# Optimization experiments

Hardware: AMD Instinct MI355X
Metric: run time of the kernel (lower is better)

## Reference

```python
import jax, jax.numpy as jnp
import numpy as np

N_EMB = 384
BLOCK_SIZE = 256


def setup_inputs() -> dict:
    key = jax.random.key(0)
    ks = jax.random.split(key, 6)
    B, T, H, D = 256, 256, 6, 64
    x = jax.random.normal(ks[0], (B, T, N_EMB), dtype=jnp.float32)
    wk = jax.random.normal(ks[1], (H, N_EMB, D), dtype=jnp.float32) * (N_EMB ** -0.5)
    wq = jax.random.normal(ks[2], (H, N_EMB, D), dtype=jnp.float32) * (N_EMB ** -0.5)
    wv = jax.random.normal(ks[3], (H, N_EMB, D), dtype=jnp.float32) * (N_EMB ** -0.5)
    wproj = jax.random.normal(ks[4], (N_EMB, N_EMB), dtype=jnp.float32) * (N_EMB ** -0.5)
    bproj = jnp.zeros((N_EMB,), dtype=jnp.float32)
    return {"x": x, "wk": wk, "wq": wq, "wv": wv, "wproj": wproj, "bproj": bproj}


def reference(x, wk, wq, wv, wproj, bproj):
    B, T, C = x.shape  # C == N_EMB
    # per-head projections (no bias), heads stacked on leading axis
    k = jnp.einsum('btc,hcd->bhtd', x, wk)
    q = jnp.einsum('btc,hcd->bhtd', x, wq)
    v = jnp.einsum('btc,hcd->bhtd', x, wv)
    # faithful to source: wei = k @ q^T scaled by sqrt(C) (embed dim, not head dim)
    wei = jnp.einsum('bhtd,bhsd->bhts', k, q) / (C ** 0.5)
    causal = jnp.tril(jnp.ones((T, T), dtype=bool))
    wei = jnp.where(causal, wei, -jnp.inf)
    wei = jax.nn.softmax(wei, axis=-1)
    # dropout is identity in eval mode
    out = jnp.einsum('bhts,bhsd->bhtd', wei, v)  # [B,H,T,D]
    out = out.transpose(0, 2, 1, 3).reshape(B, T, C)  # concat heads
    out = out @ wproj + bproj
    return out
```

## Files before the change

### kernel.cpp

```cpp
#include <hip/hip_runtime.h>

typedef unsigned short u16;
typedef __bf16 bf16x8 __attribute__((ext_vector_type(8)));
typedef float f32x4 __attribute__((ext_vector_type(4)));

#define B_SZ 256
#define T_SZ 256
#define C_EMB 384
#define NHEAD 6
#define DHEAD 64
#define N3 1152
#define BHTD 25165824
#define SCALE 0.05103103630798287f

__device__ __forceinline__ u16 f2bf(float f) {
  unsigned u = __float_as_uint(f);
  u += 0x7FFFu + ((u >> 16) & 1u);
  return (u16)(u >> 16);
}

__device__ __forceinline__ void gload_lds16(const void* g, void* l) {
  __builtin_amdgcn_global_load_lds((const __attribute__((address_space(1))) void*)g,
                                   (__attribute__((address_space(3))) void*)l, 16, 0, 0);
}

__global__ __launch_bounds__(256) void prep_weights(
    const float* __restrict__ wk, const float* __restrict__ wq,
    const float* __restrict__ wv, const float* __restrict__ wproj,
    u16* __restrict__ wqkvt, u16* __restrict__ wprojt) {
  int i = blockIdx.x * 256 + threadIdx.x;
  if (i < N3 * C_EMB) {
    int n = i / C_EMB, c = i - n * C_EMB;
    int tensor = n >= 768 ? 2 : (n >= 384 ? 1 : 0);
    int r = n - tensor * 384;
    int h = r >> 6, d = r & 63;
    const float* w = tensor == 0 ? wk : (tensor == 1 ? wq : wv);
    float val = w[(h * C_EMB + c) * DHEAD + d];
    if (tensor == 0) val *= SCALE;
    wqkvt[i] = f2bf(val);
  } else {
    int ii = i - N3 * C_EMB;
    if (ii < C_EMB * C_EMB) {
      int n = ii / C_EMB, c = ii - n * C_EMB;
      wprojt[ii] = f2bf(wproj[c * C_EMB + n]);
    }
  }
}

__global__ __launch_bounds__(256) void prep_x(const float* __restrict__ x,
                                              u16* __restrict__ xb) {
  int i = blockIdx.x * 256 + threadIdx.x;
  float4 f0 = ((const float4*)x)[i * 2];
  float4 f1 = ((const float4*)x)[i * 2 + 1];
  uint4 p;
  p.x = (unsigned)f2bf(f0.x) | ((unsigned)f2bf(f0.y) << 16);
  p.y = (unsigned)f2bf(f0.z) | ((unsigned)f2bf(f0.w) << 16);
  p.z = (unsigned)f2bf(f1.x) | ((unsigned)f2bf(f1.y) << 16);
  p.w = (unsigned)f2bf(f1.z) | ((unsigned)f2bf(f1.w) << 16);
  ((uint4*)xb)[i] = p;
}

__global__ __launch_bounds__(256) void qkv_gemm(const u16* __restrict__ xb,
                                                const u16* __restrict__ wt,
                                                u16* __restrict__ kqv) {
  __shared__ __align__(16) u16 lA[2][128 * 64];
  __shared__ __align__(16) u16 lB[2][128 * 64];
  const int tid = threadIdx.x;
  const int lane = tid & 63, w = tid >> 6;
  int bid = blockIdx.x;
  int nb = (bid & 7) * 576 + (bid >> 3);
  int mt = nb / 9, nt = nb - mt * 9;
  const int n0 = nt * 128, m0 = mt * 128;
  const int wr = w >> 1, wc = w & 1;
  f32x4 acc[4][4] = {};

#define QSTAGE(buf, kt_) { \
    int k0_ = (kt_) * 64; \
    _Pragma("unroll") for (int it = 0; it < 4; ++it) { \
      int ub = it * 256 + w * 64; int u = ub + lane; \
      int row = u >> 3, cu = u & 7; \
      int koff = k0_ + ((cu ^ (row & 7)) << 3); \
      gload_lds16(xb + (size_t)(m0 + row) * C_EMB + koff, lA[buf] + ub * 8); \
      gload_lds16(wt + (size_t)(n0 + row) * C_EMB + koff, lB[buf] + ub * 8); \
    } }

  QSTAGE(0, 0);
  int cur = 0;
  for (int kt = 0; kt < 6; ++kt) {
    if (kt < 5) {
      QSTAGE(cur ^ 1, kt + 1);
      asm volatile("s_waitcnt vmcnt(8)" ::: "memory");
    } else {
      asm volatile("s_waitcnt vmcnt(0)" ::: "memory");
    }
    asm volatile("s_barrier" ::: "memory");
    bf16x8 af[4][2], bfr[4][2];
#pragma unroll
    for (int mi = 0; mi < 4; ++mi) {
      int row = wr * 64 + mi * 16 + (lane & 15);
#pragma unroll
      for (int kk = 0; kk < 2; ++kk) {
        int cu = kk * 4 + (lane >> 4);
        af[mi][kk] = *(const bf16x8*)((const char*)lA[cur] + row * 128 + ((cu ^ (row & 7)) << 4));
      }
    }
#pragma unroll
    for (int ni = 0; ni < 4; ++ni) {
      int row = wc * 64 + ni * 16 + (lane & 15);
#pragma unroll
      for (int kk = 0; kk < 2; ++kk) {
        int cu = kk * 4 + (lane >> 4);
        bfr[ni][kk] = *(const bf16x8*)((const char*)lB[cur] + row * 128 + ((cu ^ (row & 7)) << 4));
      }
    }
#pragma unroll
    for (int kk = 0; kk < 2; ++kk)
#pragma unroll
      for (int mi = 0; mi < 4; ++mi)
#pragma unroll
        for (int ni = 0; ni < 4; ++ni)
          acc[mi][ni] = __builtin_amdgcn_mfma_f32_16x16x32_bf16(
              af[mi][kk], bfr[ni][kk], acc[mi][ni], 0, 0, 0);
    asm volatile("s_barrier" ::: "memory");
    cur ^= 1;
  }
#undef QSTAGE

  const int tensor = nt / 3;
  if (tensor == 2) {
    u16* vt = kqv + 2 * (size_t)BHTD;
#pragma unroll
    for (int ni = 0; ni < 4; ++ni) {
      int r2 = n0 + wc * 64 + ni * 16 + (lane & 15) - 768;
      int h = r2 >> 6, d = r2 & 63;
#pragma unroll
      for (int mi = 0; mi < 4; ++mi) {
        int gm0 = m0 + wr * 64 + mi * 16 + ((lane >> 4) << 2);
        int b = gm0 >> 8, tt = gm0 & 255;
        ushort4 pk;
        pk.x = f2bf(acc[mi][ni][0]);
        pk.y = f2bf(acc[mi][ni][1]);
        pk.z = f2bf(acc[mi][ni][2]);
        pk.w = f2bf(acc[mi][ni][3]);
        *(ushort4*)(vt + ((size_t)(b * NHEAD + h) * 64 + d) * 256 + tt) = pk;
      }
    }
  } else {
#pragma unroll
    for (int ni = 0; ni < 4; ++ni) {
      int gn = n0 + wc * 64 + ni * 16 + (lane & 15);
      int r2 = gn - tensor * 384;
      int h = r2 >> 6, d = r2 & 63;
#pragma unroll
      for (int mi = 0; mi < 4; ++mi) {
        int gm0 = m0 + wr * 64 + mi * 16 + ((lane >> 4) << 2);
#pragma unroll
        for (int r = 0; r < 4; ++r) {
          int m = gm0 + r;
          int b = m >> 8, t = m & 255;
          kqv[(size_t)tensor * BHTD + ((((b * NHEAD + h) << 8) + t) << 6) + d] =
              f2bf(acc[mi][ni][r]);
        }
      }
    }
  }
}

__global__ __launch_bounds__(512, 4) void attn_kernel(const u16* __restrict__ kqv,
                                                      u16* __restrict__ attnb) {
  __shared__ __align__(16) u16 lK[128 * 64];
  __shared__ __align__(16) u16 lQ[2][64 * 64];
  __shared__ __align__(16) u16 lVt[2][64 * 64];
  __shared__ __align__(16) char lP[8 * 16 * 144];
  const int tid = threadIdx.x;
  const int lane = tid & 63, w = tid >> 6;
  int bid = blockIdx.x;
  int id = (bid & 7) * 384 + (bid >> 3);
  const int bh = id >> 1, tt = id & 1;
  const int t0 = tt * 128;
  const u16* Kb = kqv + (size_t)bh * (T_SZ * DHEAD);
  const u16* Qb = kqv + (size_t)BHTD + (size_t)bh * (T_SZ * DHEAD);
  const u16* Vb = kqv + 2 * (size_t)BHTD + (size_t)bh * (DHEAD * T_SZ);

#define STAGE_Q(buf, ss) { int ub = w * 64; int u = ub + lane; \
    int row = u >> 3, cu = u & 7; \
    gload_lds16(Qb + (size_t)((ss) + row) * DHEAD + ((cu ^ (row & 7)) << 3), lQ[buf] + ub * 8); }
#define STAGE_V(buf, ss) { int ub = w * 64; int u = ub + lane; \
    int row = u >> 3, cu = u & 7; \
    gload_lds16(Vb + (size_t)row * T_SZ + (ss) + ((cu ^ (row & 7)) << 3), lVt[buf] + ub * 8); }

#pragma unroll
  for (int it = 0; it < 2; ++it) {
    int ub = it * 512 + w * 64;
    int u = ub + lane;
    int row = u >> 3, cu = u & 7;
    gload_lds16(Kb + (size_t)(t0 + row) * DHEAD + ((cu ^ (row & 7)) << 3), lK + ub * 8);
  }
  STAGE_Q(0, 0);
  STAGE_V(0, 0);
  asm volatile("s_waitcnt vmcnt(2)" ::: "memory");
  asm volatile("s_barrier" ::: "memory");

  const int t0w = t0 + w * 16;
  const int tg0 = t0w + ((lane >> 4) << 2);
  bf16x8 af[2];
  {
    int arow = w * 16 + (lane & 15);
#pragma unroll
    for (int kk = 0; kk < 2; ++kk) {
      int cu = kk * 4 + (lane >> 4);
      af[kk] = *(const bf16x8*)((const char*)lK + arow * 128 + ((cu ^ (arow & 7)) << 4));
    }
  }
  char* lPw = lP + w * (16 * 144);
  f32x4 oacc[4] = {};
  float mrow[4] = {-1e30f, -1e30f, -1e30f, -1e30f};
  float lrowp[4] = {0.f, 0.f, 0.f, 0.f};
  const int nst = 2 * tt + 2;
  int cur = 0;
  for (int si = 0; si < nst; ++si) {
    const int s0 = si << 6;
    if (si + 1 < nst) {
      STAGE_Q(cur ^ 1, s0 + 64);
      STAGE_V(cur ^ 1, s0 + 64);
      asm volatile("s_waitcnt vmcnt(2)" ::: "memory");
    } else {
      asm volatile("s_waitcnt vmcnt(0)" ::: "memory");
    }
    asm volatile("s_barrier" ::: "memory");
    if (s0 <= t0w + 15) {
      f32x4 sacc[4] = {};
#pragma unroll
      for (int ni = 0; ni < 4; ++ni) {
        int row = ni * 16 + (lane & 15);
#pragma unroll
        for (int kk = 0; kk < 2; ++kk) {
          int cu = kk * 4 + (lane >> 4);
          bf16x8 bq = *(const bf16x8*)((const char*)lQ[cur] + row * 128 + ((cu ^ (row & 7)) << 4));
          sacc[ni] = __builtin_amdgcn_mfma_f32_16x16x32_bf16(af[kk], bq, sacc[ni], 0, 0, 0);
        }
      }
      float pm[4][4];
      float rmax[4] = {-1e30f, -1e30f, -1e30f, -1e30f};
      if (s0 + 63 > t0w) {
#pragma unroll
        for (int ni = 0; ni < 4; ++ni) {
          int sg = s0 + ni * 16 + (lane & 15);
#pragma unroll
          for (int r = 0; r < 4; ++r) {
            float vv = sacc[ni][r];
            if (sg > tg0 + r) vv = -1e30f;
            pm[ni][r] = vv;
            rmax[r] = fmaxf(rmax[r], vv);
          }
        }
      } else {
#pragma unroll
        for (int ni = 0; ni < 4; ++ni)
#pragma unroll
          for (int r = 0; r < 4; ++r) {
            float vv = sacc[ni][r];
            pm[ni][r] = vv;
            rmax[r] = fmaxf(rmax[r], vv);
          }
      }
#pragma unroll
      for (int r = 0; r < 4; ++r) {
#pragma unroll
        for (int off = 1; off < 16; off <<= 1)
          rmax[r] = fmaxf(rmax[r], __shfl_xor(rmax[r], off));
      }
      bool small = (rmax[0] - mrow[0] <= 8.f) && (rmax[1] - mrow[1] <= 8.f) &&
                   (rmax[2] - mrow[2] <= 8.f) && (rmax[3] - mrow[3] <= 8.f);
      if (!__all(small)) {
#pragma unroll
        for (int r = 0; r < 4; ++r) {
          float mnew = fmaxf(mrow[r], rmax[r]);
          float alpha = __expf(mrow[r] - mnew);
          mrow[r] = mnew;
          lrowp[r] *= alpha;
#pragma unroll
          for (int nd = 0; nd < 4; ++nd) oacc[nd][r] *= alpha;
        }
      }
#pragma unroll
      for (int ni = 0; ni < 4; ++ni)
#pragma unroll
        for (int r = 0; r < 4; ++r) {
          float p = __expf(pm[ni][r] - mrow[r]);
          pm[ni][r] = p;
          lrowp[r] += p;
        }
#pragma unroll
      for (int ni = 0; ni < 4; ++ni) {
        int scol = ni * 16 + (lane & 15);
#pragma unroll
        for (int r = 0; r < 4; ++r) {
          int trow = ((lane >> 4) << 2) + r;
          *(u16*)(lPw + trow * 144 + scol * 2) = f2bf(pm[ni][r]);
        }
      }
      bf16x8 pa[2];
      {
        int trow = lane & 15;
#pragma unroll
        for (int kk = 0; kk < 2; ++kk) {
          int cu = kk * 4 + (lane >> 4);
          pa[kk] = *(const bf16x8*)(lPw + trow * 144 + cu * 16);
        }
      }
#pragma unroll
      for (int nd = 0; nd < 4; ++nd) {
        int drow = nd * 16 + (lane & 15);
#pragma unroll
        for (int kk = 0; kk < 2; ++kk) {
          int cu = kk * 4 + (lane >> 4);
          bf16x8 vb = *(const bf16x8*)((const char*)lVt[cur] + drow * 128 + ((cu ^ (drow & 7)) << 4));
          oacc[nd] = __builtin_amdgcn_mfma_f32_16x16x32_bf16(pa[kk], vb, oacc[nd], 0, 0, 0);
        }
      }
    }
    asm volatile("s_barrier" ::: "memory");
    cur ^= 1;
  }
#undef STAGE_Q
#undef STAGE_V
#pragma unroll
  for (int r = 0; r < 4; ++r) {
#pragma unroll
    for (int off = 1; off < 16; off <<= 1)
      lrowp[r] += __shfl_xor(lrowp[r], off);
  }
  const int b = bh / NHEAD, h = bh - (bh / NHEAD) * NHEAD;
#pragma unroll
  for (int r = 0; r < 4; ++r) {
    int t = tg0 + r;
    float inv = 1.0f / lrowp[r];
#pragma unroll
    for (int nd = 0; nd < 4; ++nd) {
      int col = h * 64 + nd * 16 + (lane & 15);
      attnb[((size_t)(b * T_SZ + t)) * C_EMB + col] = f2bf(oacc[nd][r] * inv);
    }
  }
}

__global__ __launch_bounds__(256) void out_gemm(const u16* __restrict__ a,
                                                const u16* __restrict__ wt,
                                                const float* __restrict__ bias,
                                                float* __restrict__ out) {
  __shared__ __align__(16) u16 lA[2][128 * 64];
  __shared__ __align__(16) u16 lB[2][128 * 64];
  const int tid = threadIdx.x;
  const int lane = tid & 63, w = tid >> 6;
  int bid = blockIdx.x;
  int nb = (bid & 7) * 192 + (bid >> 3);
  int mt = nb / 3, nt = nb - mt * 3;
  const int n0 = nt * 128, m0 = mt * 128;
  const int wr = w >> 1, wc = w & 1;
  f32x4 acc[4][4] = {};

#define OSTAGE(buf, kt_) { \
    int k0_ = (kt_) * 64; \
    _Pragma("unroll") for (int it = 0; it < 4; ++it) { \
      int ub = it * 256 + w * 64; int u = ub + lane; \
      int row = u >> 3, cu = u & 7; \
      int koff = k0_ + ((cu ^ (row & 7)) << 3); \
      gload_lds16(a + (size_t)(m0 + row) * C_EMB + koff, lA[buf] + ub * 8); \
      gload_lds16(wt + (size_t)(n0 + row) * C_EMB + koff, lB[buf] + ub * 8); \
    } }

  OSTAGE(0, 0);
  int cur = 0;
  for (int kt = 0; kt < 6; ++kt) {
    if (kt < 5) {
      OSTAGE(cur ^ 1, kt + 1);
      asm volatile("s_waitcnt vmcnt(8)" ::: "memory");
    } else {
      asm volatile("s_waitcnt vmcnt(0)" ::: "memory");
    }
    asm volatile("s_barrier" ::: "memory");
    bf16x8 af[4][2], bfr[4][2];
#pragma unroll
    for (int mi = 0; mi < 4; ++mi) {
      int row = wr * 64 + mi * 16 + (lane & 15);
#pragma unroll
      for (int kk = 0; kk < 2; ++kk) {
        int cu = kk * 4 + (lane >> 4);
        af[mi][kk] = *(const bf16x8*)((const char*)lA[cur] + row * 128 + ((cu ^ (row & 7)) << 4));
      }
    }
#pragma unroll
    for (int ni = 0; ni < 4; ++ni) {
      int row = wc * 64 + ni * 16 + (lane & 15);
#pragma unroll
      for (int kk = 0; kk < 2; ++kk) {
        int cu = kk * 4 + (lane >> 4);
        bfr[ni][kk] = *(const bf16x8*)((const char*)lB[cur] + row * 128 + ((cu ^ (row & 7)) << 4));
      }
    }
#pragma unroll
    for (int kk = 0; kk < 2; ++kk)
#pragma unroll
      for (int mi = 0; mi < 4; ++mi)
#pragma unroll
        for (int ni = 0; ni < 4; ++ni)
          acc[mi][ni] = __builtin_amdgcn_mfma_f32_16x16x32_bf16(
              af[mi][kk], bfr[ni][kk], acc[mi][ni], 0, 0, 0);
    asm volatile("s_barrier" ::: "memory");
    cur ^= 1;
  }
#undef OSTAGE
#pragma unroll
  for (int ni = 0; ni < 4; ++ni) {
    int gn = n0 + wc * 64 + ni * 16 + (lane & 15);
    float bv = bias[gn];
#pragma unroll
    for (int mi = 0; mi < 4; ++mi) {
      int gm0 = m0 + wr * 64 + mi * 16 + ((lane >> 4) << 2);
#pragma unroll
      for (int r = 0; r < 4; ++r)
        out[(size_t)(gm0 + r) * C_EMB + gn] = acc[mi][ni][r] + bv;
    }
  }
}

extern "C" void kernel_launch(void* const* d_in, const int* in_sizes, int n_in,
                              void* d_out, int out_size, void* d_ws, size_t ws_size,
                              hipStream_t stream) {
  const float* x = (const float*)d_in[0];
  const float* wk = (const float*)d_in[1];
  const float* wq = (const float*)d_in[2];
  const float* wv = (const float*)d_in[3];
  const float* wproj = (const float*)d_in[4];
  const float* bproj = (const float*)d_in[5];
  float* out = (float*)d_out;
  u16* ws = (u16*)d_ws;
  u16* kqv = ws;
  u16* attnb = ws + 3 * (size_t)BHTD;
  u16* xb = attnb;
  u16* wqkvt = attnb + (size_t)BHTD;
  u16* wprojt = wqkvt + (size_t)N3 * C_EMB;
  prep_weights<<<2304, 256, 0, stream>>>(wk, wq, wv, wproj, wqkvt, wprojt);
  prep_x<<<12288, 256, 0, stream>>>(x, xb);
  qkv_gemm<<<4608, 256, 0, stream>>>(xb, wqkvt, kqv);
  attn_kernel<<<3072, 512, 0, stream>>>(kqv, attnb);
  out_gemm<<<1536, 256, 0, stream>>>(attnb, wprojt, bproj, out);
}
```

Baseline: 206.8 us.

## Merge prep kernels, drop GEMM double buffering, load K directly, fuse softmax masking

Merges the two preprocessing kernels into a single launch. Both GEMMs drop LDS double buffering for a single buffer with launch bounds allowing 4 blocks per CU, so occupancy is meant to hide memory latency instead of software pipelining. The attention kernel loads K fragments straight from global memory into registers, removing the K LDS tile and raising the occupancy hint to 6. It also fuses the causal mask into the exp/store pass so the pm temporary array is no longer needed. The GEMMs lose load/compute overlap within a block, which could hurt if occupancy does not actually rise.

```diff
diff --git a/kernel.cpp b/kernel.cpp
--- a/kernel.cpp
+++ b/kernel.cpp
@@ -24,47 +24,48 @@
                                    (__attribute__((address_space(3))) void*)l, 16, 0, 0);
 }
 
-__global__ __launch_bounds__(256) void prep_weights(
-    const float* __restrict__ wk, const float* __restrict__ wq,
-    const float* __restrict__ wv, const float* __restrict__ wproj,
-    u16* __restrict__ wqkvt, u16* __restrict__ wprojt) {
-  int i = blockIdx.x * 256 + threadIdx.x;
-  if (i < N3 * C_EMB) {
-    int n = i / C_EMB, c = i - n * C_EMB;
-    int tensor = n >= 768 ? 2 : (n >= 384 ? 1 : 0);
-    int r = n - tensor * 384;
-    int h = r >> 6, d = r & 63;
-    const float* w = tensor == 0 ? wk : (tensor == 1 ? wq : wv);
-    float val = w[(h * C_EMB + c) * DHEAD + d];
-    if (tensor == 0) val *= SCALE;
-    wqkvt[i] = f2bf(val);
+__global__ __launch_bounds__(256) void prep_all(
+    const float* __restrict__ x, const float* __restrict__ wk,
+    const float* __restrict__ wq, const float* __restrict__ wv,
+    const float* __restrict__ wproj,
+    u16* __restrict__ xb, u16* __restrict__ wqkvt, u16* __restrict__ wprojt) {
+  int bidx = blockIdx.x;
+  if (bidx < 12288) {
+    int i = bidx * 256 + threadIdx.x;
+    float4 f0 = ((const float4*)x)[i * 2];
+    float4 f1 = ((const float4*)x)[i * 2 + 1];
+    uint4 p;
+    p.x = (unsigned)f2bf(f0.x) | ((unsigned)f2bf(f0.y) << 16);
+    p.y = (unsigned)f2bf(f0.z) | ((unsigned)f2bf(f0.w) << 16);
+    p.z = (unsigned)f2bf(f1.x) | ((unsigned)f2bf(f1.y) << 16);
+    p.w = (unsigned)f2bf(f1.z) | ((unsigned)f2bf(f1.w) << 16);
+    ((uint4*)xb)[i] = p;
   } else {
-    int ii = i - N3 * C_EMB;
-    if (ii < C_EMB * C_EMB) {
-      int n = ii / C_EMB, c = ii - n * C_EMB;
-      wprojt[ii] = f2bf(wproj[c * C_EMB + n]);
-    }
-  }
-}
-
-__global__ __launch_bounds__(256) void prep_x(const float* __restrict__ x,
-                                              u16* __restrict__ xb) {
-  int i = blockIdx.x * 256 + threadIdx.x;
-  float4 f0 = ((const float4*)x)[i * 2];
-  float4 f1 = ((const float4*)x)[i * 2 + 1];
-  uint4 p;
-  p.x = (unsigned)f2bf(f0.x) | ((unsigned)f2bf(f0.y) << 16);
-  p.y = (unsigned)f2bf(f0.z) | ((unsigned)f2bf(f0.w) << 16);
-  p.z = (unsigned)f2bf(f1.x) | ((unsigned)f2bf(f1.y) << 16);
-  p.w = (unsigned)f2bf(f1.z) | ((unsigned)f2bf(f1.w) << 16);
-  ((uint4*)xb)[i] = p;
-}
-
-__global__ __launch_bounds__(256) void qkv_gemm(const u16* __restrict__ xb,
-                                                const u16* __restrict__ wt,
-                                                u16* __restrict__ kqv) {
-  __shared__ __align__(16) u16 lA[2][128 * 64];
-  __shared__ __align__(16) u16 lB[2][128 * 64];
+    int i = (bidx - 12288) * 256 + threadIdx.x;
+    if (i < N3 * C_EMB) {
+      int n = i / C_EMB, c = i - n * C_EMB;
+      int tensor = n >= 768 ? 2 : (n >= 384 ? 1 : 0);
+      int r = n - tensor * 384;
+      int h = r >> 6, d = r & 63;
+      const float* w = tensor == 0 ? wk : (tensor == 1 ? wq : wv);
+      float val = w[(h * C_EMB + c) * DHEAD + d];
+      if (tensor == 0) val *= SCALE;
+      wqkvt[i] = f2bf(val);
+    } else {
+      int ii = i - N3 * C_EMB;
+      if (ii < C_EMB * C_EMB) {
+        int n = ii / C_EMB, c = ii - n * C_EMB;
+        wprojt[ii] = f2bf(wproj[c * C_EMB + n]);
+      }
+    }
+  }
+}
+
+__global__ __launch_bounds__(256, 4) void qkv_gemm(const u16* __restrict__ xb,
+                                                   const u16* __restrict__ wt,
+                                                   u16* __restrict__ kqv) {
+  __shared__ __align__(16) u16 lA[128 * 64];
+  __shared__ __align__(16) u16 lB[128 * 64];
   const int tid = threadIdx.x;
   const int lane = tid & 63, w = tid >> 6;
   int bid = blockIdx.x;
@@ -73,26 +74,18 @@
   const int n0 = nt * 128, m0 = mt * 128;
   const int wr = w >> 1, wc = w & 1;
   f32x4 acc[4][4] = {};
-
-#define QSTAGE(buf, kt_) { \
-    int k0_ = (kt_) * 64; \
-    _Pragma("unroll") for (int it = 0; it < 4; ++it) { \
-      int ub = it * 256 + w * 64; int u = ub + lane; \
-      int row = u >> 3, cu = u & 7; \
-      int koff = k0_ + ((cu ^ (row & 7)) << 3); \
-      gload_lds16(xb + (size_t)(m0 + row) * C_EMB + koff, lA[buf] + ub * 8); \
-      gload_lds16(wt + (size_t)(n0 + row) * C_EMB + koff, lB[buf] + ub * 8); \
-    } }
-
-  QSTAGE(0, 0);
-  int cur = 0;
   for (int kt = 0; kt < 6; ++kt) {
-    if (kt < 5) {
-      QSTAGE(cur ^ 1, kt + 1);
-      asm volatile("s_waitcnt vmcnt(8)" ::: "memory");
-    } else {
-      asm volatile("s_waitcnt vmcnt(0)" ::: "memory");
-    }
+    const int k0 = kt * 64;
+#pragma unroll
+    for (int it = 0; it < 4; ++it) {
+      int ub = it * 256 + w * 64;
+      int u = ub + lane;
+      int row = u >> 3, cu = u & 7;
+      int koff = k0 + ((cu ^ (row & 7)) << 3);
+      gload_lds16(xb + (size_t)(m0 + row) * C_EMB + koff, lA + ub * 8);
+      gload_lds16(wt + (size_t)(n0 + row) * C_EMB + koff, lB + ub * 8);
+    }
+    asm volatile("s_waitcnt vmcnt(0)" ::: "memory");
     asm volatile("s_barrier" ::: "memory");
     bf16x8 af[4][2], bfr[4][2];
 #pragma unroll
@@ -101,7 +94,7 @@
 #pragma unroll
       for (int kk = 0; kk < 2; ++kk) {
         int cu = kk * 4 + (lane >> 4);
-        af[mi][kk] = *(const bf16x8*)((const char*)lA[cur] + row * 128 + ((cu ^ (row & 7)) << 4));
+        af[mi][kk] = *(const bf16x8*)((const char*)lA + row * 128 + ((cu ^ (row & 7)) << 4));
       }
     }
 #pragma unroll
@@ -110,7 +103,7 @@
 #pragma unroll
       for (int kk = 0; kk < 2; ++kk) {
         int cu = kk * 4 + (lane >> 4);
-        bfr[ni][kk] = *(const bf16x8*)((const char*)lB[cur] + row * 128 + ((cu ^ (row & 7)) << 4));
+        bfr[ni][kk] = *(const bf16x8*)((const char*)lB + row * 128 + ((cu ^ (row & 7)) << 4));
       }
     }
 #pragma unroll
@@ -122,9 +115,7 @@
           acc[mi][ni] = __builtin_amdgcn_mfma_f32_16x16x32_bf16(
               af[mi][kk], bfr[ni][kk], acc[mi][ni], 0, 0, 0);
     asm volatile("s_barrier" ::: "memory");
-    cur ^= 1;
-  }
-#undef QSTAGE
+  }
 
   const int tensor = nt / 3;
   if (tensor == 2) {
@@ -136,13 +127,13 @@
 #pragma unroll
       for (int mi = 0; mi < 4; ++mi) {
         int gm0 = m0 + wr * 64 + mi * 16 + ((lane >> 4) << 2);
-        int b = gm0 >> 8, tt = gm0 & 255;
+        int b = gm0 >> 8, tt2 = gm0 & 255;
         ushort4 pk;
         pk.x = f2bf(acc[mi][ni][0]);
         pk.y = f2bf(acc[mi][ni][1]);
         pk.z = f2bf(acc[mi][ni][2]);
         pk.w = f2bf(acc[mi][ni][3]);
-        *(ushort4*)(vt + ((size_t)(b * NHEAD + h) * 64 + d) * 256 + tt) = pk;
+        *(ushort4*)(vt + ((size_t)(b * NHEAD + h) * 64 + d) * 256 + tt2) = pk;
       }
     }
   } else {
@@ -166,9 +157,8 @@
   }
 }
 
-__global__ __launch_bounds__(512, 4) void attn_kernel(const u16* __restrict__ kqv,
+__global__ __launch_bounds__(512, 6) void attn_kernel(const u16* __restrict__ kqv,
                                                       u16* __restrict__ attnb) {
-  __shared__ __align__(16) u16 lK[128 * 64];
   __shared__ __align__(16) u16 lQ[2][64 * 64];
   __shared__ __align__(16) u16 lVt[2][64 * 64];
   __shared__ __align__(16) char lP[8 * 16 * 144];
@@ -189,29 +179,19 @@
     int row = u >> 3, cu = u & 7; \
     gload_lds16(Vb + (size_t)row * T_SZ + (ss) + ((cu ^ (row & 7)) << 3), lVt[buf] + ub * 8); }
 
-#pragma unroll
-  for (int it = 0; it < 2; ++it) {
-    int ub = it * 512 + w * 64;
-    int u = ub + lane;
-    int row = u >> 3, cu = u & 7;
-    gload_lds16(Kb + (size_t)(t0 + row) * DHEAD + ((cu ^ (row & 7)) << 3), lK + ub * 8);
-  }
+  const int t0w = t0 + w * 16;
+  const int tg0 = t0w + ((lane >> 4) << 2);
   STAGE_Q(0, 0);
   STAGE_V(0, 0);
+  bf16x8 af[2];
+  {
+    const u16* kr = Kb + (size_t)(t0w + (lane & 15)) * DHEAD;
+    af[0] = *(const bf16x8*)(kr + ((lane >> 4) << 3));
+    af[1] = *(const bf16x8*)(kr + 32 + ((lane >> 4) << 3));
+  }
   asm volatile("s_waitcnt vmcnt(2)" ::: "memory");
   asm volatile("s_barrier" ::: "memory");
 
-  const int t0w = t0 + w * 16;
-  const int tg0 = t0w + ((lane >> 4) << 2);
-  bf16x8 af[2];
-  {
-    int arow = w * 16 + (lane & 15);
-#pragma unroll
-    for (int kk = 0; kk < 2; ++kk) {
-      int cu = kk * 4 + (lane >> 4);
-      af[kk] = *(const bf16x8*)((const char*)lK + arow * 128 + ((cu ^ (arow & 7)) << 4));
-    }
-  }
   char* lPw = lP + w * (16 * 144);
   f32x4 oacc[4] = {};
   float mrow[4] = {-1e30f, -1e30f, -1e30f, -1e30f};
@@ -240,29 +220,22 @@
           sacc[ni] = __builtin_amdgcn_mfma_f32_16x16x32_bf16(af[kk], bq, sacc[ni], 0, 0, 0);
         }
       }
-      float pm[4][4];
+      const bool diag = (s0 + 63 > t0w);
       float rmax[4] = {-1e30f, -1e30f, -1e30f, -1e30f};
-      if (s0 + 63 > t0w) {
+      if (diag) {
 #pragma unroll
         for (int ni = 0; ni < 4; ++ni) {
           int sg = s0 + ni * 16 + (lane & 15);
 #pragma unroll
-          for (int r = 0; r < 4; ++r) {
-            float vv = sacc[ni][r];
-            if (sg > tg0 + r) vv = -1e30f;
-            pm[ni][r] = vv;
-            rmax[r] = fmaxf(rmax[r], vv);
-          }
+          for (int r = 0; r < 4; ++r)
+            rmax[r] = fmaxf(rmax[r], (sg > tg0 + r) ? -1e30f : sacc[ni][r]);
         }
       } else {
 #pragma unroll
         for (int ni = 0; ni < 4; ++ni)
 #pragma unroll
-          for (int r = 0; r < 4; ++r) {
-            float vv = sacc[ni][r];
-            pm[ni][r] = vv;
-            rmax[r] = fmaxf(rmax[r], vv);
-          }
+          for (int r = 0; r < 4; ++r)
+            rmax[r] = fmaxf(rmax[r], sacc[ni][r]);
       }
 #pragma unroll
       for (int r = 0; r < 4; ++r) {
@@ -283,21 +256,31 @@
           for (int nd = 0; nd < 4; ++nd) oacc[nd][r] *= alpha;
         }
       }
-#pragma unroll
-      for (int ni = 0; ni < 4; ++ni)
-#pragma unroll
-        for (int r = 0; r < 4; ++r) {
-          float p = __expf(pm[ni][r] - mrow[r]);
-          pm[ni][r] = p;
-          lrowp[r] += p;
-        }
-#pragma unroll
-      for (int ni = 0; ni < 4; ++ni) {
-        int scol = ni * 16 + (lane & 15);
-#pragma unroll
-        for (int r = 0; r < 4; ++r) {
-          int trow = ((lane >> 4) << 2) + r;
-          *(u16*)(lPw + trow * 144 + scol * 2) = f2bf(pm[ni][r]);
+      if (diag) {
+#pragma unroll
+        for (int ni = 0; ni < 4; ++ni) {
+          int sg = s0 + ni * 16 + (lane & 15);
+          int scol = ni * 16 + (lane & 15);
+#pragma unroll
+          for (int r = 0; r < 4; ++r) {
+            float p = __expf(sacc[ni][r] - mrow[r]);
+            p = (sg > tg0 + r) ? 0.f : p;
+            lrowp[r] += p;
+            int trow = ((lane >> 4) << 2) + r;
+            *(u16*)(lPw + trow * 144 + scol * 2) = f2bf(p);
+          }
+        }
+      } else {
+#pragma unroll
+        for (int ni = 0; ni < 4; ++ni) {
+          int scol = ni * 16 + (lane & 15);
+#pragma unroll
+          for (int r = 0; r < 4; ++r) {
+            float p = __expf(sacc[ni][r] - mrow[r]);
+            lrowp[r] += p;
+            int trow = ((lane >> 4) << 2) + r;
+            *(u16*)(lPw + trow * 144 + scol * 2) = f2bf(p);
+          }
         }
       }
       bf16x8 pa[2];
@@ -344,12 +327,12 @@
   }
 }
 
-__global__ __launch_bounds__(256) void out_gemm(const u16* __restrict__ a,
-                                                const u16* __restrict__ wt,
-                                                const float* __restrict__ bias,
-                                                float* __restrict__ out) {
-  __shared__ __align__(16) u16 lA[2][128 * 64];
-  __shared__ __align__(16) u16 lB[2][128 * 64];
+__global__ __launch_bounds__(256, 4) void out_gemm(const u16* __restrict__ a,
+                                                   const u16* __restrict__ wt,
+                                                   const float* __restrict__ bias,
+                                                   float* __restrict__ out) {
+  __shared__ __align__(16) u16 lA[128 * 64];
+  __shared__ __align__(16) u16 lB[128 * 64];
   const int tid = threadIdx.x;
   const int lane = tid & 63, w = tid >> 6;
   int bid = blockIdx.x;
@@ -358,26 +341,18 @@
   const int n0 = nt * 128, m0 = mt * 128;
   const int wr = w >> 1, wc = w & 1;
   f32x4 acc[4][4] = {};
-
-#define OSTAGE(buf, kt_) { \
-    int k0_ = (kt_) * 64; \
-    _Pragma("unroll") for (int it = 0; it < 4; ++it) { \
-      int ub = it * 256 + w * 64; int u = ub + lane; \
-      int row = u >> 3, cu = u & 7; \
-      int koff = k0_ + ((cu ^ (row & 7)) << 3); \
-      gload_lds16(a + (size_t)(m0 + row) * C_EMB + koff, lA[buf] + ub * 8); \
-      gload_lds16(wt + (size_t)(n0 + row) * C_EMB + koff, lB[buf] + ub * 8); \
-    } }
-
-  OSTAGE(0, 0);
-  int cur = 0;
   for (int kt = 0; kt < 6; ++kt) {
-    if (kt < 5) {
-      OSTAGE(cur ^ 1, kt + 1);
-      asm volatile("s_waitcnt vmcnt(8)" ::: "memory");
-    } else {
-      asm volatile("s_waitcnt vmcnt(0)" ::: "memory");
-    }
+    const int k0 = kt * 64;
+#pragma unroll
+    for (int it = 0; it < 4; ++it) {
+      int ub = it * 256 + w * 64;
+      int u = ub + lane;
+      int row = u >> 3, cu = u & 7;
+      int koff = k0 + ((cu ^ (row & 7)) << 3);
+      gload_lds16(a + (size_t)(m0 + row) * C_EMB + koff, lA + ub * 8);
+      gload_lds16(wt + (size_t)(n0 + row) * C_EMB + koff, lB + ub * 8);
+    }
+    asm volatile("s_waitcnt vmcnt(0)" ::: "memory");
     asm volatile("s_barrier" ::: "memory");
     bf16x8 af[4][2], bfr[4][2];
 #pragma unroll
@@ -386,7 +361,7 @@
 #pragma unroll
       for (int kk = 0; kk < 2; ++kk) {
         int cu = kk * 4 + (lane >> 4);
-        af[mi][kk] = *(const bf16x8*)((const char*)lA[cur] + row * 128 + ((cu ^ (row & 7)) << 4));
+        af[mi][kk] = *(const bf16x8*)((const char*)lA + row * 128 + ((cu ^ (row & 7)) << 4));
       }
     }
 #pragma unroll
@@ -395,7 +370,7 @@
 #pragma unroll
       for (int kk = 0; kk < 2; ++kk) {
         int cu = kk * 4 + (lane >> 4);
-        bfr[ni][kk] = *(const bf16x8*)((const char*)lB[cur] + row * 128 + ((cu ^ (row & 7)) << 4));
+        bfr[ni][kk] = *(const bf16x8*)((const char*)lB + row * 128 + ((cu ^ (row & 7)) << 4));
       }
     }
 #pragma unroll
@@ -407,9 +382,7 @@
           acc[mi][ni] = __builtin_amdgcn_mfma_f32_16x16x32_bf16(
               af[mi][kk], bfr[ni][kk], acc[mi][ni], 0, 0, 0);
     asm volatile("s_barrier" ::: "memory");
-    cur ^= 1;
-  }
-#undef OSTAGE
+  }
 #pragma unroll
   for (int ni = 0; ni < 4; ++ni) {
     int gn = n0 + wc * 64 + ni * 16 + (lane & 15);
@@ -440,8 +413,7 @@
   u16* xb = attnb;
   u16* wqkvt = attnb + (size_t)BHTD;
   u16* wprojt = wqkvt + (size_t)N3 * C_EMB;
-  prep_weights<<<2304, 256, 0, stream>>>(wk, wq, wv, wproj, wqkvt, wprojt);
-  prep_x<<<12288, 256, 0, stream>>>(x, xb);
+  prep_all<<<14592, 256, 0, stream>>>(x, wk, wq, wv, wproj, xb, wqkvt, wprojt);
   qkv_gemm<<<4608, 256, 0, stream>>>(xb, wqkvt, kqv);
   attn_kernel<<<3072, 512, 0, stream>>>(kqv, attnb);
   out_gemm<<<1536, 256, 0, stream>>>(attnb, wprojt, bproj, out);
```

After: 202.8 us. About the same (-1.9%).
